# Optimization experiments

Measured on AMD Instinct MI355X. Metric: run time of the kernel, lower is better.

The kernel has to match this reference:

```python
import jax, jax.numpy as jnp
import numpy as np

N, D, H, C = 4096, 4096, 256, 16
NNZ_ATTR, E, NNZ_JM, NNZ_JA = 262144, 131072, 400000, 80000


def setup_inputs() -> dict:
    key = jax.random.key(0)
    ks = jax.random.split(key, 8)
    return {
        "attr_row": jax.random.randint(ks[0], (NNZ_ATTR,), 0, N),
        "attr_col": jax.random.randint(ks[1], (NNZ_ATTR,), 0, D),
        "edge_idx": jax.random.randint(ks[2], (2, E), 0, N),
        "j_mask_idx": jax.random.randint(ks[3], (2, NNZ_JM), 0, N),
        "jaug_mask_idx": jax.random.randint(ks[4], (2, NNZ_JA), 0, N),
        "lin1_w": jax.random.normal(ks[5], (H, D), dtype=jnp.float32) * (1.0 / np.sqrt(D)),
        "lin2_w": jax.random.normal(ks[6], (C, H), dtype=jnp.float32) * (1.0 / np.sqrt(H)),
        "bias2": jax.random.normal(ks[7], (C,), dtype=jnp.float32) * 0.01,
        "n": N,
        "d": D,
    }


def _gcn_norm_dense(a, n):
    # add remaining self loops (binary adjacency -> set diagonal to 1)
    idx = jnp.arange(n)
    a = a.at[idx, idx].set(1.0)
    # PyG gcn_norm: deg = scatter_add(weight, col) = column sums
    deg = a.sum(axis=0)
    dinv = jnp.where(deg > 0, jax.lax.rsqrt(deg), 0.0)
    # out[i] = sum_j dinv[i]*dinv[j]*A[j,i]*x[j]  ->  An = Dinv @ A^T @ Dinv
    return (dinv[:, None] * a.T) * dinv[None, :]


def reference(attr_row, attr_col, edge_idx, j_mask_idx, jaug_mask_idx,
              lin1_w, lin2_w, bias2, n, d):
    # --- edge augmentation: (edges AND J_mask) OR JAug_mask ---
    a = jnp.zeros((n, n), jnp.float32).at[edge_idx[0], edge_idx[1]].set(1.0)
    jm = jnp.zeros((n, n), bool).at[j_mask_idx[0], j_mask_idx[1]].set(True)
    ja = jnp.zeros((n, n), bool).at[jaug_mask_idx[0], jaug_mask_idx[1]].set(True)
    a_aug = jnp.maximum(jnp.where(jm, a, 0.0), ja.astype(jnp.float32))

    # --- layer 1: spmm(sparse binary X, W1^T), gcn_norm, propagate (no bias) ---
    x = jnp.zeros((n, d), jnp.float32).at[attr_row, attr_col].add(1.0)
    h = x @ lin1_w.T                     # [n, H]
    an = _gcn_norm_dense(a_aug, n)       # [n, n] normalized adjacency
    h = jax.nn.relu(an @ h)              # propagate + relu
    # dropout is identity in eval mode

    # --- layer 2: standard GCNConv with bias ---
    h2 = h @ lin2_w.T                    # [n, C]
    out = an @ h2 + bias2
    return out
```

## Files before the change

### kernel.cpp

```cpp
#include <hip/hip_runtime.h>

#define N_      4096
#define D_      4096
#define H_      256
#define C_      16
#define NNZ_ATTR 262144
#define E_      131072
#define NNZ_JM  400000
#define NNZ_JA  80000
#define WORDS   128
#define ADJ_STRIDE 128
#define ASTR    128
#define NT      256

#define OFF_EBT  ((size_t)0)
#define OFF_JMT  ((size_t)(2u<<20))
#define OFF_JAT  ((size_t)(4u<<20))
#define OFF_CNT  ((size_t)(6u<<20))
#define OFF_DINV (OFF_CNT + (size_t)(16u<<10))
#define OFF_DEG  (OFF_CNT + (size_t)(32u<<10))
#define OFF_CCOL (OFF_CNT + (size_t)(48u<<10))
#define OFF_ADJ  (OFF_CCOL + (size_t)(2u<<20))
#define OFF_W1T  (OFF_ADJ + (size_t)(2u<<20))
#define OFF_H1   (OFF_W1T + (size_t)(4u<<20))
#define OFF_H2   (OFF_H1  + (size_t)(4u<<20))

#define ZERO_BYTES (OFF_CNT + (size_t)(16u<<10))
#define ZB_BLOCKS  1540
#define TR_BLOCKS  1024
#define SC_ITEMS   (E_ + NNZ_JM + NNZ_JA + NNZ_ATTR)
#define SC_BLOCKS  (SC_ITEMS / NT)

__global__ void k_pre(const float* __restrict__ w1, float* __restrict__ w1t,
                      uint4* __restrict__ zp) {
    __shared__ float tile[32][33];
    int b = blockIdx.x, t = threadIdx.x;
    if (b < ZB_BLOCKS) {
        zp[(size_t)b * NT + t] = make_uint4(0u, 0u, 0u, 0u);
    } else {
        int bb = b - ZB_BLOCKS;
        int gx = bb & 127, gy = bb >> 7;
        int tx = t & 31, ty = t >> 5;
        int col = gx * 32 + tx;
        #pragma unroll
        for (int j = 0; j < 4; ++j)
            tile[ty + j * 8][tx] = w1[(size_t)(gy * 32 + ty + j * 8) * D_ + col];
        __syncthreads();
        int ocol = gy * 32 + tx;
        #pragma unroll
        for (int j = 0; j < 4; ++j)
            w1t[(size_t)(gx * 32 + ty + j * 8) * H_ + ocol] = tile[tx][ty + j * 8];
    }
}

__global__ void k_scatter(const int* __restrict__ attr_row, const int* __restrict__ attr_col,
                          const int* __restrict__ edge, const int* __restrict__ jmsk,
                          const int* __restrict__ jaug,
                          unsigned* __restrict__ ebt, unsigned* __restrict__ jmt,
                          unsigned* __restrict__ jat, unsigned* __restrict__ cnt,
                          unsigned* __restrict__ ccol) {
    int i = blockIdx.x * NT + threadIdx.x;
    if (i < E_) {
        int p = edge[i], q = edge[E_ + i];
        atomicOr(&ebt[(size_t)q * WORDS + (p >> 5)], 1u << (p & 31));
    } else if (i < E_ + NNZ_JM) {
        int j = i - E_;
        int p = jmsk[j], q = jmsk[NNZ_JM + j];
        atomicOr(&jmt[(size_t)q * WORDS + (p >> 5)], 1u << (p & 31));
    } else if (i < E_ + NNZ_JM + NNZ_JA) {
        int j = i - E_ - NNZ_JM;
        int p = jaug[j], q = jaug[NNZ_JA + j];
        atomicOr(&jat[(size_t)q * WORDS + (p >> 5)], 1u << (p & 31));
    } else {
        int j = i - E_ - NNZ_JM - NNZ_JA;
        int r = attr_row[j];
        unsigned pos = atomicAdd(&cnt[r], 1u);
        if (pos < ASTR) ccol[(size_t)r * ASTR + pos] = (unsigned)attr_col[j];
    }
}

__global__ void k_rowh1(const unsigned* __restrict__ ebt, const unsigned* __restrict__ jmt,
                        const unsigned* __restrict__ jat, const unsigned* __restrict__ cnt,
                        const unsigned* __restrict__ ccol, const float* __restrict__ w1t,
                        float* __restrict__ dinv, int* __restrict__ deg,
                        int* __restrict__ adj, float* __restrict__ h1s) {
    __shared__ __align__(16) char smem[4640];
    unsigned* cols = (unsigned*)smem;
    float* part = (float*)(smem + 512);
    float* sdinv = (float*)(smem + 512 + 4096);
    const int b = blockIdx.x, t = threadIdx.x;
    int wv = t >> 6, lane = t & 63;
    int q = 4 * b + wv;
    {
        const uint2* er = (const uint2*)(ebt + (size_t)q * WORDS);
        const uint2* jr = (const uint2*)(jmt + (size_t)q * WORDS);
        const uint2* ar = (const uint2*)(jat + (size_t)q * WORDS);
        uint2 e2 = er[lane], j2 = jr[lane], a2 = ar[lane];
        unsigned w0 = (e2.x & j2.x) | a2.x;
        unsigned w1b = (e2.y & j2.y) | a2.y;
        int dw = q >> 5;
        if ((dw >> 1) == lane) {
            if (dw & 1) w1b |= 1u << (q & 31); else w0 |= 1u << (q & 31);
        }
        int c = __popc(w0) + __popc(w1b);
        int pre = c;
        #pragma unroll
        for (int d2 = 1; d2 < 64; d2 <<= 1) {
            int x = __shfl_up(pre, d2);
            if (lane >= d2) pre += x;
        }
        int excl = pre - c;
        int total = __shfl(pre, 63);
        if (lane == 0) {
            float dv = rsqrtf((float)total);
            dinv[q] = dv;
            sdinv[wv] = dv;
            deg[q] = total < ADJ_STRIDE ? total : ADJ_STRIDE;
        }
        unsigned idx = (unsigned)excl;
        int* arow = adj + (size_t)q * ADJ_STRIDE;
        int base0 = lane * 64;
        while (w0)  { int bp = __ffs(w0) - 1;  w0  &= w0 - 1;  if (idx < ADJ_STRIDE) arow[idx] = base0 + bp;      ++idx; }
        while (w1b) { int bp = __ffs(w1b) - 1; w1b &= w1b - 1; if (idx < ADJ_STRIDE) arow[idx] = base0 + 32 + bp; ++idx; }
    }
    __syncthreads();
    int g = t >> 6;
    for (int i = 0; i < 4; ++i) {
        int r = 4 * b + i;
        unsigned m = min(cnt[r], (unsigned)ASTR);
        if ((unsigned)t < m) cols[t] = ccol[(size_t)r * ASTR + t];
        __syncthreads();
        float4 acc = make_float4(0.f, 0.f, 0.f, 0.f);
        unsigned j = (unsigned)g;
        for (; j + 12 < m; j += 16) {
            unsigned c0 = cols[j], c1 = cols[j + 4], c2 = cols[j + 8], c3 = cols[j + 12];
            float4 v0 = *(const float4*)&w1t[(size_t)c0 * H_ + lane * 4];
            float4 v1 = *(const float4*)&w1t[(size_t)c1 * H_ + lane * 4];
            float4 v2 = *(const float4*)&w1t[(size_t)c2 * H_ + lane * 4];
            float4 v3 = *(const float4*)&w1t[(size_t)c3 * H_ + lane * 4];
            acc.x += v0.x + v1.x + v2.x + v3.x;
            acc.y += v0.y + v1.y + v2.y + v3.y;
            acc.z += v0.z + v1.z + v2.z + v3.z;
            acc.w += v0.w + v1.w + v2.w + v3.w;
        }
        for (; j < m; j += 4) {
            unsigned c0 = cols[j];
            float4 v0 = *(const float4*)&w1t[(size_t)c0 * H_ + lane * 4];
            acc.x += v0.x; acc.y += v0.y; acc.z += v0.z; acc.w += v0.w;
        }
        ((float4*)part)[g * 64 + lane] = acc;
        __syncthreads();
        int comp = t & 3, idx4 = t >> 2;
        float s0 = part[(0 * 64 + idx4) * 4 + comp];
        float s1 = part[(1 * 64 + idx4) * 4 + comp];
        float s2 = part[(2 * 64 + idx4) * 4 + comp];
        float s3 = part[(3 * 64 + idx4) * 4 + comp];
        h1s[(size_t)r * H_ + t] = (s0 + s1 + s2 + s3) * sdinv[i];
        __syncthreads();
    }
}

__global__ void k_prop1(const int* __restrict__ adj, const int* __restrict__ deg,
                        const float* __restrict__ dinv, const float* __restrict__ h1s,
                        const float* __restrict__ w2, float* __restrict__ h2s) {
    __shared__ __align__(16) char smem[2688];
    int* adj_s = (int*)smem;
    float* hrow = (float*)(smem + 512);
    float* partial = (float*)(smem + 512 + 1024);
    const int b = blockIdx.x, t = threadIdx.x;
    int c = t & 15, g = t >> 4;
    float w2r[16];
    #pragma unroll
    for (int kk = 0; kk < 16; ++kk) w2r[kk] = w2[(size_t)c * H_ + g * 16 + kk];
    for (int i = 0; i < 4; ++i) {
        int q = 4 * b + i;
        __syncthreads();
        if (t < ADJ_STRIDE) adj_s[t] = adj[(size_t)q * ADJ_STRIDE + t];
        __syncthreads();
        int dg = deg[q];
        float acc = 0.f;
        int j = 0;
        for (; j + 4 <= dg; j += 4) {
            int p0 = adj_s[j], p1 = adj_s[j + 1], p2 = adj_s[j + 2], p3 = adj_s[j + 3];
            acc += h1s[(size_t)p0 * H_ + t] + h1s[(size_t)p1 * H_ + t]
                 + h1s[(size_t)p2 * H_ + t] + h1s[(size_t)p3 * H_ + t];
        }
        for (; j < dg; ++j) acc += h1s[(size_t)adj_s[j] * H_ + t];
        float dq = dinv[q];
        hrow[t] = fmaxf(acc * dq, 0.f);
        __syncthreads();
        float part = 0.f;
        #pragma unroll
        for (int kk = 0; kk < 16; ++kk) part += hrow[g * 16 + kk] * w2r[kk];
        partial[g * 17 + c] = part;
        __syncthreads();
        if (t < 16) {
            float s = 0.f;
            #pragma unroll
            for (int g2 = 0; g2 < 16; ++g2) s += partial[g2 * 17 + t];
            h2s[(size_t)q * C_ + t] = s * dq;
        }
    }
}

__global__ void k_prop2(const int* __restrict__ adj, const int* __restrict__ deg,
                        const float* __restrict__ dinv, const float* __restrict__ h2s,
                        const float* __restrict__ bias, float* __restrict__ out) {
    const int b = blockIdx.x, t = threadIdx.x;
    int wv = t >> 6, lane = t & 63;
    int q = 4 * b + wv;
    int c = lane & 15, prt = lane >> 4;
    int dg = deg[q];
    const int* arow = adj + (size_t)q * ADJ_STRIDE;
    float acc = 0.f;
    for (int j = prt; j < dg; j += 4)
        acc += h2s[(size_t)arow[j] * C_ + c];
    acc += __shfl_down(acc, 32);
    acc += __shfl_down(acc, 16);
    if (lane < 16)
        out[(size_t)q * C_ + c] = dinv[q] * acc + bias[c];
}


extern "C" void kernel_launch(void* const* d_in, const int* in_sizes, int n_in,
                              void* d_out, int out_size, void* d_ws, size_t ws_size,
                              hipStream_t stream) {
    const int*   attr_row = (const int*)d_in[0];
    const int*   attr_col = (const int*)d_in[1];
    const int*   edge     = (const int*)d_in[2];
    const int*   jmsk     = (const int*)d_in[3];
    const int*   jaug     = (const int*)d_in[4];
    const float* w1       = (const float*)d_in[5];
    const float* w2       = (const float*)d_in[6];
    const float* bias2    = (const float*)d_in[7];
    float*       out      = (float*)d_out;

    char* ws = (char*)d_ws;
    unsigned* ebt  = (unsigned*)(ws + OFF_EBT);
    unsigned* jmt  = (unsigned*)(ws + OFF_JMT);
    unsigned* jat  = (unsigned*)(ws + OFF_JAT);
    unsigned* cnt  = (unsigned*)(ws + OFF_CNT);
    float*    dinv = (float*)(ws + OFF_DINV);
    int*      deg  = (int*)(ws + OFF_DEG);
    unsigned* ccol = (unsigned*)(ws + OFF_CCOL);
    int*      adj  = (int*)(ws + OFF_ADJ);
    float*    w1t  = (float*)(ws + OFF_W1T);
    float*    h1s  = (float*)(ws + OFF_H1);
    float*    h2s  = (float*)(ws + OFF_H2);

    k_pre<<<ZB_BLOCKS + TR_BLOCKS, NT, 0, stream>>>(w1, w1t, (uint4*)d_ws);
    k_scatter<<<SC_BLOCKS, NT, 0, stream>>>(attr_row, attr_col, edge, jmsk, jaug,
                                            ebt, jmt, jat, cnt, ccol);
    k_rowh1<<<N_ / 4, NT, 0, stream>>>(ebt, jmt, jat, cnt, ccol, w1t,
                                       dinv, deg, adj, h1s);
    k_prop1<<<N_ / 4, NT, 0, stream>>>(adj, deg, dinv, h1s, w2, h2s);
    k_prop2<<<N_ / 4, NT, 0, stream>>>(adj, deg, dinv, h2s, bias2, out);
}
```

Baseline: 92.46 us.

## Build augmented adjacency bitmap directly, filtering J-mask scatter by edge bitmap

Replaces the three separate bitmaps (edges, J-mask, JAug-mask) with two. JAug entries and the self-loop diagonal are scattered straight into one combined bitmap, and a second pass ORs in J-mask entries only where the edge bit is set. This shrinks the zeroing and reading of one 2MB bitmap, skips atomics for J-mask entries with no edge, and removes the three-way combine in k_rowh1. In exchange it adds a kernel launch and a dependent pass, and moves the zeroing into its own kernel.

```diff
diff --git a/kernel.cpp b/kernel.cpp
--- a/kernel.cpp
+++ b/kernel.cpp
@@ -14,9 +14,8 @@
 #define NT      256
 
 #define OFF_EBT  ((size_t)0)
-#define OFF_JMT  ((size_t)(2u<<20))
-#define OFF_JAT  ((size_t)(4u<<20))
-#define OFF_CNT  ((size_t)(6u<<20))
+#define OFF_ABT  ((size_t)(2u<<20))
+#define OFF_CNT  ((size_t)(4u<<20))
 #define OFF_DINV (OFF_CNT + (size_t)(16u<<10))
 #define OFF_DEG  (OFF_CNT + (size_t)(32u<<10))
 #define OFF_CCOL (OFF_CNT + (size_t)(48u<<10))
@@ -26,19 +25,47 @@
 #define OFF_H2   (OFF_H1  + (size_t)(4u<<20))
 
 #define ZERO_BYTES (OFF_CNT + (size_t)(16u<<10))
-#define ZB_BLOCKS  1540
-#define TR_BLOCKS  1024
-#define SC_ITEMS   (E_ + NNZ_JM + NNZ_JA + NNZ_ATTR)
-#define SC_BLOCKS  (SC_ITEMS / NT)
-
-__global__ void k_pre(const float* __restrict__ w1, float* __restrict__ w1t,
-                      uint4* __restrict__ zp) {
+#define ZB_BLOCKS  1028
+
+#define SB_ATTR  0
+#define SB_EDGE  1024
+#define SB_JA    1536
+#define SB_DIAG  1849
+#define SB_TR    1865
+#define SB_TOTAL 2889
+
+__global__ void k_zero(uint4* __restrict__ zp) {
+    zp[(size_t)blockIdx.x * NT + threadIdx.x] = make_uint4(0u, 0u, 0u, 0u);
+}
+
+__global__ void k_scat1(const int* __restrict__ attr_row, const int* __restrict__ attr_col,
+                        const int* __restrict__ edge, const int* __restrict__ jaug,
+                        const float* __restrict__ w1,
+                        unsigned* __restrict__ ebt, unsigned* __restrict__ abt,
+                        unsigned* __restrict__ cnt, unsigned* __restrict__ ccol,
+                        float* __restrict__ w1t) {
     __shared__ float tile[32][33];
-    int b = blockIdx.x, t = threadIdx.x;
-    if (b < ZB_BLOCKS) {
-        zp[(size_t)b * NT + t] = make_uint4(0u, 0u, 0u, 0u);
+    const int b = blockIdx.x, t = threadIdx.x;
+    if (b < SB_EDGE) {
+        int i = b * NT + t;
+        int r = attr_row[i];
+        unsigned pos = atomicAdd(&cnt[r], 1u);
+        if (pos < ASTR) ccol[(size_t)r * ASTR + pos] = (unsigned)attr_col[i];
+    } else if (b < SB_JA) {
+        int j = (b - SB_EDGE) * NT + t;
+        int p = edge[j], q = edge[E_ + j];
+        atomicOr(&ebt[(size_t)q * WORDS + (p >> 5)], 1u << (p & 31));
+    } else if (b < SB_DIAG) {
+        int j = (b - SB_JA) * NT + t;
+        if (j < NNZ_JA) {
+            int p = jaug[j], q = jaug[NNZ_JA + j];
+            atomicOr(&abt[(size_t)q * WORDS + (p >> 5)], 1u << (p & 31));
+        }
+    } else if (b < SB_TR) {
+        int r = (b - SB_DIAG) * NT + t;
+        atomicOr(&abt[(size_t)r * WORDS + (r >> 5)], 1u << (r & 31));
     } else {
-        int bb = b - ZB_BLOCKS;
+        int bb = b - SB_TR;
         int gx = bb & 127, gy = bb >> 7;
         int tx = t & 31, ty = t >> 5;
         int col = gx * 32 + tx;
@@ -53,34 +80,17 @@
     }
 }
 
-__global__ void k_scatter(const int* __restrict__ attr_row, const int* __restrict__ attr_col,
-                          const int* __restrict__ edge, const int* __restrict__ jmsk,
-                          const int* __restrict__ jaug,
-                          unsigned* __restrict__ ebt, unsigned* __restrict__ jmt,
-                          unsigned* __restrict__ jat, unsigned* __restrict__ cnt,
-                          unsigned* __restrict__ ccol) {
+__global__ void k_scat2(const int* __restrict__ jmsk,
+                        const unsigned* __restrict__ ebt, unsigned* __restrict__ abt) {
     int i = blockIdx.x * NT + threadIdx.x;
-    if (i < E_) {
-        int p = edge[i], q = edge[E_ + i];
-        atomicOr(&ebt[(size_t)q * WORDS + (p >> 5)], 1u << (p & 31));
-    } else if (i < E_ + NNZ_JM) {
-        int j = i - E_;
-        int p = jmsk[j], q = jmsk[NNZ_JM + j];
-        atomicOr(&jmt[(size_t)q * WORDS + (p >> 5)], 1u << (p & 31));
-    } else if (i < E_ + NNZ_JM + NNZ_JA) {
-        int j = i - E_ - NNZ_JM;
-        int p = jaug[j], q = jaug[NNZ_JA + j];
-        atomicOr(&jat[(size_t)q * WORDS + (p >> 5)], 1u << (p & 31));
-    } else {
-        int j = i - E_ - NNZ_JM - NNZ_JA;
-        int r = attr_row[j];
-        unsigned pos = atomicAdd(&cnt[r], 1u);
-        if (pos < ASTR) ccol[(size_t)r * ASTR + pos] = (unsigned)attr_col[j];
-    }
-}
-
-__global__ void k_rowh1(const unsigned* __restrict__ ebt, const unsigned* __restrict__ jmt,
-                        const unsigned* __restrict__ jat, const unsigned* __restrict__ cnt,
+    if (i >= NNZ_JM) return;
+    int p = jmsk[i], q = jmsk[NNZ_JM + i];
+    size_t w = (size_t)q * WORDS + (p >> 5);
+    if ((ebt[w] >> (p & 31)) & 1u)
+        atomicOr(&abt[w], 1u << (p & 31));
+}
+
+__global__ void k_rowh1(const unsigned* __restrict__ abt, const unsigned* __restrict__ cnt,
                         const unsigned* __restrict__ ccol, const float* __restrict__ w1t,
                         float* __restrict__ dinv, int* __restrict__ deg,
                         int* __restrict__ adj, float* __restrict__ h1s) {
@@ -92,16 +102,8 @@
     int wv = t >> 6, lane = t & 63;
     int q = 4 * b + wv;
     {
-        const uint2* er = (const uint2*)(ebt + (size_t)q * WORDS);
-        const uint2* jr = (const uint2*)(jmt + (size_t)q * WORDS);
-        const uint2* ar = (const uint2*)(jat + (size_t)q * WORDS);
-        uint2 e2 = er[lane], j2 = jr[lane], a2 = ar[lane];
-        unsigned w0 = (e2.x & j2.x) | a2.x;
-        unsigned w1b = (e2.y & j2.y) | a2.y;
-        int dw = q >> 5;
-        if ((dw >> 1) == lane) {
-            if (dw & 1) w1b |= 1u << (q & 31); else w0 |= 1u << (q & 31);
-        }
+        uint2 m2 = ((const uint2*)(abt + (size_t)q * WORDS))[lane];
+        unsigned w0 = m2.x, w1b = m2.y;
         int c = __popc(w0) + __popc(w1b);
         int pre = c;
         #pragma unroll
@@ -237,8 +239,7 @@
 
     char* ws = (char*)d_ws;
     unsigned* ebt  = (unsigned*)(ws + OFF_EBT);
-    unsigned* jmt  = (unsigned*)(ws + OFF_JMT);
-    unsigned* jat  = (unsigned*)(ws + OFF_JAT);
+    unsigned* abt  = (unsigned*)(ws + OFF_ABT);
     unsigned* cnt  = (unsigned*)(ws + OFF_CNT);
     float*    dinv = (float*)(ws + OFF_DINV);
     int*      deg  = (int*)(ws + OFF_DEG);
@@ -248,11 +249,11 @@
     float*    h1s  = (float*)(ws + OFF_H1);
     float*    h2s  = (float*)(ws + OFF_H2);
 
-    k_pre<<<ZB_BLOCKS + TR_BLOCKS, NT, 0, stream>>>(w1, w1t, (uint4*)d_ws);
-    k_scatter<<<SC_BLOCKS, NT, 0, stream>>>(attr_row, attr_col, edge, jmsk, jaug,
-                                            ebt, jmt, jat, cnt, ccol);
-    k_rowh1<<<N_ / 4, NT, 0, stream>>>(ebt, jmt, jat, cnt, ccol, w1t,
-                                       dinv, deg, adj, h1s);
+    k_zero<<<ZB_BLOCKS, NT, 0, stream>>>((uint4*)d_ws);
+    k_scat1<<<SB_TOTAL, NT, 0, stream>>>(attr_row, attr_col, edge, jaug, w1,
+                                         ebt, abt, cnt, ccol, w1t);
+    k_scat2<<<(NNZ_JM + NT - 1) / NT, NT, 0, stream>>>(jmsk, ebt, abt);
+    k_rowh1<<<N_ / 4, NT, 0, stream>>>(abt, cnt, ccol, w1t, dinv, deg, adj, h1s);
     k_prop1<<<N_ / 4, NT, 0, stream>>>(adj, deg, dinv, h1s, w2, h2s);
     k_prop2<<<N_ / 4, NT, 0, stream>>>(adj, deg, dinv, h2s, bias2, out);
 }
```

Measured after the change: 81.51 us. -11.8%, faster.
